# Optimization experiments

Measured on AMD Instinct MI355X. Metric: run time of the kernel, lower is better.

The kernel has to match this reference:

```python
import jax, jax.numpy as jnp
import numpy as np
from jax import lax

WIDTH = 1.0  # hysteresis play-operator width (init kwarg)


def setup_inputs() -> dict:
    key = jax.random.key(0)
    k1, k2 = jax.random.split(key)
    T = 16777216  # sequence length
    x = jax.random.normal(k1, (T,), dtype=jnp.float32)
    state = jnp.zeros((), dtype=jnp.float32)  # scalar initial state
    kernel = jax.random.normal(k2, (), dtype=jnp.float32)  # scalar learned weight
    return {"x": x, "state": state, "kernel": kernel}


def reference(x, state, kernel):
    # y[t] = kernel * x[t]
    # out[t] = Phi(y[t] - out[t-1], width) + out[t-1], out[-1] = state
    # Phi(z) = max(z, 0) + min(z + width, 0)
    y = kernel * x

    def step(carry, yt):
        z = yt - carry
        out = jnp.maximum(z, 0.0) + jnp.minimum(z + WIDTH, 0.0) + carry
        return out, out

    _, outs = lax.scan(step, state, y)
    return outs
```

## Files before the change

kernel.cpp:

```cpp
#include <hip/hip_runtime.h>


#define T_LEN   16777216
#define NTH     256
#define WIN     256
#define NWIN    4
#define UNIT    (WIN * NWIN)
#define NU      (T_LEN / UNIT)
#define NBLK    (NU / 4)
#define WPLAY   1.0f

__device__ __forceinline__ void combine(float La, float Ha, float Lb, float Hb,
                                        float& Lo, float& Ho) {
    Lo = fminf(fmaxf(La, Lb), Hb);
    Ho = fminf(fmaxf(Ha, Lb), Hb);
}

__global__ __launch_bounds__(NTH, 4) void playscan(const float* __restrict__ x,
                                                   const float* __restrict__ kptr,
                                                   const float* __restrict__ s0ptr,
                                                   float* __restrict__ out) {
    const float k  = kptr[0];
    const float s0 = s0ptr[0];
    const int lane = threadIdx.x & 63;
    const int wid  = threadIdx.x >> 6;
    const int unit = blockIdx.x * 4 + wid;
    const long ubase = (long)unit * UNIT;

    float4 v[NWIN];
#pragma unroll
    for (int w = 0; w < NWIN; ++w)
        v[w] = *(const float4*)(x + ubase + (long)w * WIN + lane * 4);

    float rL[NWIN * 4], rH[NWIN * 4];
    float UL = -INFINITY, UH = INFINITY;
#pragma unroll
    for (int w = 0; w < NWIN; ++w) {
        float pL[4], pH[4];
        float L = -INFINITY, H = INFINITY, y;
        y = k * v[w].x; L = fminf(fmaxf(L, y), y + WPLAY); H = fminf(fmaxf(H, y), y + WPLAY); pL[0] = L; pH[0] = H;
        y = k * v[w].y; L = fminf(fmaxf(L, y), y + WPLAY); H = fminf(fmaxf(H, y), y + WPLAY); pL[1] = L; pH[1] = H;
        y = k * v[w].z; L = fminf(fmaxf(L, y), y + WPLAY); H = fminf(fmaxf(H, y), y + WPLAY); pL[2] = L; pH[2] = H;
        y = k * v[w].w; L = fminf(fmaxf(L, y), y + WPLAY); H = fminf(fmaxf(H, y), y + WPLAY); pL[3] = L; pH[3] = H;

#pragma unroll
        for (int d = 1; d < 64; d <<= 1) {
            float Lp = __shfl_up(L, d);
            float Hp = __shfl_up(H, d);
            float Ln, Hn; combine(Lp, Hp, L, H, Ln, Hn);
            if (lane >= d) { L = Ln; H = Hn; }
        }
        float eL = __shfl_up(L, 1), eH = __shfl_up(H, 1);
        if (lane == 0) { eL = -INFINITY; eH = INFINITY; }
        float AL = __shfl(L, 63), AH = __shfl(H, 63);

        float ceL, ceH; combine(UL, UH, eL, eH, ceL, ceH);
#pragma unroll
        for (int i = 0; i < 4; ++i)
            combine(ceL, ceH, pL[i], pH[i], rL[w * 4 + i], rH[w * 4 + i]);

        { float nL, nH; combine(UL, UH, AL, AH, nL, nH); UL = nL; UH = nH; }
    }

    float s;
    if (unit == 0) {
        s = s0;
    } else {
        float accL = -INFINITY, accH = INFINITY;
        long j = (long)unit * NWIN - 1;
        while (true) {
            const float* wp = x + j * WIN;
            float4 hv = *(const float4*)(wp + lane * 4);
            float L = -INFINITY, H = INFINITY, y;
            y = k * hv.x; L = fminf(fmaxf(L, y), y + WPLAY); H = fminf(fmaxf(H, y), y + WPLAY);
            y = k * hv.y; L = fminf(fmaxf(L, y), y + WPLAY); H = fminf(fmaxf(H, y), y + WPLAY);
            y = k * hv.z; L = fminf(fmaxf(L, y), y + WPLAY); H = fminf(fmaxf(H, y), y + WPLAY);
            y = k * hv.w; L = fminf(fmaxf(L, y), y + WPLAY); H = fminf(fmaxf(H, y), y + WPLAY);
#pragma unroll
            for (int d = 1; d < 64; d <<= 1) {
                float Lp = __shfl_xor(L, d);
                float Hp = __shfl_xor(H, d);
                float Ln, Hn;
                if (lane & d) combine(Lp, Hp, L, H, Ln, Hn);
                else          combine(L, H, Lp, Hp, Ln, Hn);
                L = Ln; H = Hn;
            }
            { float nL, nH; combine(L, H, accL, accH, nL, nH); accL = nL; accH = nH; }
            if (accL == accH) { s = accL; break; }
            if (--j < 0) { s = fminf(fmaxf(s0, accL), accH); break; }
        }
    }

#pragma unroll
    for (int w = 0; w < NWIN; ++w) {
        float4 o;
        o.x = fminf(fmaxf(s, rL[w * 4 + 0]), rH[w * 4 + 0]);
        o.y = fminf(fmaxf(s, rL[w * 4 + 1]), rH[w * 4 + 1]);
        o.z = fminf(fmaxf(s, rL[w * 4 + 2]), rH[w * 4 + 2]);
        o.w = fminf(fmaxf(s, rL[w * 4 + 3]), rH[w * 4 + 3]);
        *(float4*)(out + ubase + (long)w * WIN + lane * 4) = o;
    }
}

extern "C" void kernel_launch(void* const* d_in, const int* in_sizes, int n_in,
                              void* d_out, int out_size, void* d_ws, size_t ws_size,
                              hipStream_t stream) {
    const float* x  = (const float*)d_in[0];
    const float* st = (const float*)d_in[1];
    const float* kn = (const float*)d_in[2];
    float* out = (float*)d_out;

    playscan<<<NBLK, NTH, 0, stream>>>(x, kn, st, out);
}
```

Baseline: 29.95 us.

## Share one backward walk per block and prefix wave aggregates via LDS

Only wave 0 of each block walks backward to find the block's starting state. The other waves get their entry state by composing the clamp aggregates of earlier waves, which are passed through shared memory. This removes three of four redundant backward walks and their global reads. The first walk window is prefetched before the local scan, and output stores become nontemporal. In exchange it adds two __syncthreads, and waves 1-3 sit idle while wave 0 walks.

```diff
diff --git a/kernel.cpp b/kernel.cpp
--- a/kernel.cpp
+++ b/kernel.cpp
@@ -8,7 +8,10 @@
 #define UNIT    (WIN * NWIN)
 #define NU      (T_LEN / UNIT)
 #define NBLK    (NU / 4)
+#define BWINS   (4 * NWIN)
 #define WPLAY   1.0f
+
+typedef float f32x4 __attribute__((ext_vector_type(4)));
 
 __device__ __forceinline__ void combine(float La, float Ha, float Lb, float Hb,
                                         float& Lo, float& Ho) {
@@ -26,6 +29,12 @@
     const int wid  = threadIdx.x >> 6;
     const int unit = blockIdx.x * 4 + wid;
     const long ubase = (long)unit * UNIT;
+
+    const bool walker = (wid == 0) && (blockIdx.x > 0);
+    long j = (long)blockIdx.x * BWINS - 1;
+
+    float4 hv;
+    if (walker) hv = *(const float4*)(x + j * WIN + lane * 4);
 
     float4 v[NWIN];
 #pragma unroll
@@ -62,43 +71,53 @@
         { float nL, nH; combine(UL, UH, AL, AH, nL, nH); UL = nL; UH = nH; }
     }
 
-    float s;
-    if (unit == 0) {
-        s = s0;
-    } else {
-        float accL = -INFINITY, accH = INFINITY;
-        long j = (long)unit * NWIN - 1;
-        while (true) {
-            const float* wp = x + j * WIN;
-            float4 hv = *(const float4*)(wp + lane * 4);
-            float L = -INFINITY, H = INFINITY, y;
-            y = k * hv.x; L = fminf(fmaxf(L, y), y + WPLAY); H = fminf(fmaxf(H, y), y + WPLAY);
-            y = k * hv.y; L = fminf(fmaxf(L, y), y + WPLAY); H = fminf(fmaxf(H, y), y + WPLAY);
-            y = k * hv.z; L = fminf(fmaxf(L, y), y + WPLAY); H = fminf(fmaxf(H, y), y + WPLAY);
-            y = k * hv.w; L = fminf(fmaxf(L, y), y + WPLAY); H = fminf(fmaxf(H, y), y + WPLAY);
+    __shared__ float aL[4], aH[4];
+    __shared__ float sBs;
+    if (lane == 0) { aL[wid] = UL; aH[wid] = UH; }
+    __syncthreads();
+
+    if (wid == 0) {
+        float sB;
+        if (blockIdx.x == 0) {
+            sB = s0;
+        } else {
+            float accL = -INFINITY, accH = INFINITY;
+            while (true) {
+                float L = -INFINITY, H = INFINITY, y;
+                y = k * hv.x; L = fminf(fmaxf(L, y), y + WPLAY); H = fminf(fmaxf(H, y), y + WPLAY);
+                y = k * hv.y; L = fminf(fmaxf(L, y), y + WPLAY); H = fminf(fmaxf(H, y), y + WPLAY);
+                y = k * hv.z; L = fminf(fmaxf(L, y), y + WPLAY); H = fminf(fmaxf(H, y), y + WPLAY);
+                y = k * hv.w; L = fminf(fmaxf(L, y), y + WPLAY); H = fminf(fmaxf(H, y), y + WPLAY);
 #pragma unroll
-            for (int d = 1; d < 64; d <<= 1) {
-                float Lp = __shfl_xor(L, d);
-                float Hp = __shfl_xor(H, d);
-                float Ln, Hn;
-                if (lane & d) combine(Lp, Hp, L, H, Ln, Hn);
-                else          combine(L, H, Lp, Hp, Ln, Hn);
-                L = Ln; H = Hn;
+                for (int d = 1; d < 64; d <<= 1) {
+                    float Lp = __shfl_xor(L, d);
+                    float Hp = __shfl_xor(H, d);
+                    float Ln, Hn;
+                    if (lane & d) combine(Lp, Hp, L, H, Ln, Hn);
+                    else          combine(L, H, Lp, Hp, Ln, Hn);
+                    L = Ln; H = Hn;
+                }
+                { float nL, nH; combine(L, H, accL, accH, nL, nH); accL = nL; accH = nH; }
+                if (accL == accH) { sB = accL; break; }
+                if (--j < 0)      { sB = fminf(fmaxf(s0, accL), accH); break; }
+                hv = *(const float4*)(x + j * WIN + lane * 4);
             }
-            { float nL, nH; combine(L, H, accL, accH, nL, nH); accL = nL; accH = nH; }
-            if (accL == accH) { s = accL; break; }
-            if (--j < 0) { s = fminf(fmaxf(s0, accL), accH); break; }
         }
+        if (lane == 0) sBs = sB;
     }
+    __syncthreads();
+
+    float s = sBs;
+    for (int w = 0; w < wid; ++w) s = fminf(fmaxf(s, aL[w]), aH[w]);
 
 #pragma unroll
     for (int w = 0; w < NWIN; ++w) {
-        float4 o;
+        f32x4 o;
         o.x = fminf(fmaxf(s, rL[w * 4 + 0]), rH[w * 4 + 0]);
         o.y = fminf(fmaxf(s, rL[w * 4 + 1]), rH[w * 4 + 1]);
         o.z = fminf(fmaxf(s, rL[w * 4 + 2]), rH[w * 4 + 2]);
         o.w = fminf(fmaxf(s, rL[w * 4 + 3]), rH[w * 4 + 3]);
-        *(float4*)(out + ubase + (long)w * WIN + lane * 4) = o;
+        __builtin_nontemporal_store(o, (f32x4*)(out + ubase + (long)w * WIN + lane * 4));
     }
 }
 
```

New measurement: 29.40 us. Within noise of the previous version (-1.8%).
